# Kernel tuning notes

Hardware: AMD Instinct MI355X
Metric: run time of the kernel (lower is better)

The kernel has to match this reference:

```python
import jax, jax.numpy as jnp
import numpy as np

MARGIN = 0.1
WEIGHT_BCE = 1.0
WEIGHT_SIM = 1.0
B, L = 8192, 1024


def setup_inputs() -> dict:
    key = jax.random.key(0)
    k1, k2, k3, k4 = jax.random.split(key, 4)
    # scores must be valid probabilities for BCELoss
    scores = jax.random.uniform(k1, (B, L), dtype=jnp.float32, minval=1e-4, maxval=1.0 - 1e-4)
    candidate_lengths = jax.random.randint(k2, (B,), 1, L + 1)  # int, >=1
    # exactly one positive label per sample, at a random valid index
    pos_idx = (jax.random.uniform(k3, (B,)) * candidate_lengths.astype(jnp.float32)).astype(jnp.int32)
    labels = jnp.zeros((B, L), dtype=jnp.float32).at[jnp.arange(B), pos_idx].set(1.0)
    similarity_top_cand = jax.random.normal(k4, (B,), dtype=jnp.float32)
    return {
        "scores": scores,
        "candidate_lengths": candidate_lengths,
        "labels": labels,
        "similarity_top_cand": similarity_top_cand,
    }


def reference(scores, candidate_lengths, labels, similarity_top_cand):
    max_cand_len = scores.shape[1]
    idx = jnp.arange(max_cand_len)
    mask = (idx[None, :] < candidate_lengths[:, None])  # [B, L] bool
    maskf = mask.astype(scores.dtype)

    # ---- BinaryCELoss (torch BCELoss clamps log at -100) ----
    log_p = jnp.clip(jnp.log(scores), -100.0)
    log_1mp = jnp.clip(jnp.log1p(-scores), -100.0)
    bce_el = -(labels * log_p + (1.0 - labels) * log_1mp)  # [B, L]
    # faithful to original: .mean(1) then divided again by mask.sum(1)
    bce_per = (bce_el * maskf).mean(axis=1) / maskf.sum(axis=1)
    bce_loss = bce_per.mean()

    # ---- HingeRankLoss (vectorized; one positive per sample assumption) ----
    pos_mask = maskf * (labels == 1.0)
    neg_mask = maskf * (labels == 0.0)
    pos_sum = pos_mask.sum(axis=1)              # number of positives in valid range
    neg_cnt = neg_mask.sum(axis=1)
    # chosen score: the (single) positive's score, else -margin if no positive
    chosen = jnp.where(pos_sum > 0, (scores * pos_mask).sum(axis=1), -MARGIN)  # [B]
    hinge_el = jnp.maximum(MARGIN + scores - chosen[:, None], 0.0) * neg_mask   # [B, L]
    valid = (candidate_lengths > 0) & (neg_cnt > 0)
    per_sample = jnp.where(valid, hinge_el.sum(axis=1) / jnp.maximum(neg_cnt, 1.0), 0.0)
    vcnt = valid.sum().astype(scores.dtype)
    hinge_loss = jnp.where(vcnt > 0, per_sample.sum() / jnp.maximum(vcnt, 1.0), 0.0)

    # ---- similarity loss ----
    sim_loss = -similarity_top_cand.mean()

    combined = hinge_loss + WEIGHT_BCE * bce_loss + WEIGHT_SIM * sim_loss
    return (combined, hinge_loss, bce_loss, sim_loss)
```

## Files before the change

kernel.cpp:

```cpp
#include <hip/hip_runtime.h>

#define MARGIN 0.1f

__device__ __forceinline__ float wave_sum(float v) {
    #pragma unroll
    for (int o = 32; o > 0; o >>= 1) v += __shfl_down(v, o, 64);
    return v;
}

__global__ __launch_bounds__(256) void row_kernel(
    const float* __restrict__ scores,
    const int*   __restrict__ lens,
    const float* __restrict__ labels,
    float4* __restrict__ ws_part)
{
    const int b    = blockIdx.x;
    const int t    = threadIdx.x;
    const int lane = t & 63;
    const int wave = t >> 6;
    const int len  = lens[b];

    const float4 s4 = reinterpret_cast<const float4*>(scores + (size_t)b * 1024)[t];
    const float4 l4 = reinterpret_cast<const float4*>(labels + (size_t)b * 1024)[t];
    const float sv[4] = {s4.x, s4.y, s4.z, s4.w};
    const float lv[4] = {l4.x, l4.y, l4.z, l4.w};
    const int base = t * 4;

    float bce = 0.f, pos_cnt = 0.f, pos_sum = 0.f;
    #pragma unroll
    for (int j = 0; j < 4; ++j) {
        const float m   = (base + j < len) ? 1.f : 0.f;
        const float s   = sv[j];
        const float lab = lv[j];
        const float arg = fmaf(lab, 2.f * s - 1.f, 1.f - s);
        bce     -= m * __logf(arg);
        pos_cnt += m * lab;
        pos_sum += m * lab * s;
    }

    __shared__ float red[3][4];
    bce     = wave_sum(bce);
    pos_cnt = wave_sum(pos_cnt);
    pos_sum = wave_sum(pos_sum);
    if (lane == 0) {
        red[0][wave] = bce;
        red[1][wave] = pos_cnt;
        red[2][wave] = pos_sum;
    }
    __syncthreads();
    const float bce_tot = red[0][0] + red[0][1] + red[0][2] + red[0][3];
    const float pc      = red[1][0] + red[1][1] + red[1][2] + red[1][3];
    const float ps      = red[2][0] + red[2][1] + red[2][2] + red[2][3];
    const float chosen  = (pc > 0.f) ? ps : -MARGIN;
    const float nc      = (float)len - pc;

    float hinge = 0.f;
    #pragma unroll
    for (int j = 0; j < 4; ++j) {
        const float m = (base + j < len) ? 1.f : 0.f;
        hinge += m * (1.f - lv[j]) * fmaxf(MARGIN + sv[j] - chosen, 0.f);
    }
    hinge = wave_sum(hinge);
    __shared__ float hred[4];
    if (lane == 0) hred[wave] = hinge;
    __syncthreads();

    if (t == 0) {
        const float h_tot = hred[0] + hred[1] + hred[2] + hred[3];
        const float bce_per = bce_tot * (1.f / 1024.f) / (float)len;
        const bool  valid   = (len > 0) && (nc > 0.f);
        const float h_per   = valid ? h_tot / fmaxf(nc, 1.f) : 0.f;
        ws_part[b] = make_float4(bce_per, h_per, valid ? 1.f : 0.f, 0.f);
    }
}

__global__ __launch_bounds__(256) void finalize_kernel(
    const float4* __restrict__ ws_part,
    const float*  __restrict__ sim,
    float* __restrict__ out,
    int B)
{
    const int t    = threadIdx.x;
    const int lane = t & 63;
    const int wave = t >> 6;

    float b_acc = 0.f, h_acc = 0.f, v_acc = 0.f, s_acc = 0.f;
    for (int i = t; i < B; i += 256) {
        const float4 p = ws_part[i];
        b_acc += p.x;
        h_acc += p.y;
        v_acc += p.z;
        s_acc += sim[i];
    }
    b_acc = wave_sum(b_acc);
    h_acc = wave_sum(h_acc);
    v_acc = wave_sum(v_acc);
    s_acc = wave_sum(s_acc);

    __shared__ float red[4][4];
    if (lane == 0) {
        red[0][wave] = b_acc;
        red[1][wave] = h_acc;
        red[2][wave] = v_acc;
        red[3][wave] = s_acc;
    }
    __syncthreads();

    if (t == 0) {
        const float b_tot = red[0][0] + red[0][1] + red[0][2] + red[0][3];
        const float h_tot = red[1][0] + red[1][1] + red[1][2] + red[1][3];
        const float v_tot = red[2][0] + red[2][1] + red[2][2] + red[2][3];
        const float s_tot = red[3][0] + red[3][1] + red[3][2] + red[3][3];

        const float bce_loss   = b_tot / (float)B;
        const float hinge_loss = (v_tot > 0.f) ? h_tot / fmaxf(v_tot, 1.f) : 0.f;
        const float sim_loss   = -s_tot / (float)B;

        out[0] = hinge_loss + bce_loss + sim_loss;
        out[1] = hinge_loss;
        out[2] = bce_loss;
        out[3] = sim_loss;
    }
}

extern "C" void kernel_launch(void* const* d_in, const int* in_sizes, int n_in,
                              void* d_out, int out_size, void* d_ws, size_t ws_size,
                              hipStream_t stream) {
    const float* scores = (const float*)d_in[0];
    const int*   lens   = (const int*)d_in[1];
    const float* labels = (const float*)d_in[2];
    const float* sim    = (const float*)d_in[3];
    float* out = (float*)d_out;

    const int B = in_sizes[1];

    float4* ws_part = (float4*)d_ws;

    row_kernel<<<B, 256, 0, stream>>>(scores, lens, labels, ws_part);
    finalize_kernel<<<1, 256, 0, stream>>>(ws_part, sim, out, B);
}
```

Measured before the change: 105.1 us.

## Map one wavefront per row to drop block-level syncs and LDS reductions

The row kernel now assigns each 64-lane wavefront a full row of 1024 elements (16 per lane) and packs four rows per block. All reductions become wave shuffles, which removes the two __syncthreads and the shared-memory exchanges, and the positive count is inferred from pos_sum > 0 on the assumption of a single positive per row. The sim value is folded into the per-row workspace, and the finalize kernel widens to 1024 threads. The pos_sum shortcut is a semantic assumption: it gives a wrong count if the positive score is 0 or if there are multiple positives, and each lane now holds more registers.

```diff
diff --git a/kernel.cpp b/kernel.cpp
--- a/kernel.cpp
+++ b/kernel.cpp
@@ -12,71 +12,69 @@
     const float* __restrict__ scores,
     const int*   __restrict__ lens,
     const float* __restrict__ labels,
+    const float* __restrict__ sim,
     float4* __restrict__ ws_part)
 {
-    const int b    = blockIdx.x;
-    const int t    = threadIdx.x;
-    const int lane = t & 63;
-    const int wave = t >> 6;
-    const int len  = lens[b];
+    const int lane = threadIdx.x & 63;
+    const int wave = threadIdx.x >> 6;
+    const int row  = blockIdx.x * 4 + wave;
+    const int len  = lens[row];
 
-    const float4 s4 = reinterpret_cast<const float4*>(scores + (size_t)b * 1024)[t];
-    const float4 l4 = reinterpret_cast<const float4*>(labels + (size_t)b * 1024)[t];
-    const float sv[4] = {s4.x, s4.y, s4.z, s4.w};
-    const float lv[4] = {l4.x, l4.y, l4.z, l4.w};
-    const int base = t * 4;
+    const float4* srow = reinterpret_cast<const float4*>(scores + (size_t)row * 1024);
+    const float4* lrow = reinterpret_cast<const float4*>(labels + (size_t)row * 1024);
 
-    float bce = 0.f, pos_cnt = 0.f, pos_sum = 0.f;
+    float sv[16], lv[16];
     #pragma unroll
-    for (int j = 0; j < 4; ++j) {
-        const float m   = (base + j < len) ? 1.f : 0.f;
-        const float s   = sv[j];
-        const float lab = lv[j];
-        const float arg = fmaf(lab, 2.f * s - 1.f, 1.f - s);
-        bce     -= m * __logf(arg);
-        pos_cnt += m * lab;
-        pos_sum += m * lab * s;
+    for (int k = 0; k < 4; ++k) {
+        const float4 s4 = srow[k * 64 + lane];
+        const float4 l4 = lrow[k * 64 + lane];
+        sv[k*4+0] = s4.x; sv[k*4+1] = s4.y; sv[k*4+2] = s4.z; sv[k*4+3] = s4.w;
+        lv[k*4+0] = l4.x; lv[k*4+1] = l4.y; lv[k*4+2] = l4.z; lv[k*4+3] = l4.w;
     }
 
-    __shared__ float red[3][4];
+    float bce = 0.f, pos_sum = 0.f;
+    #pragma unroll
+    for (int k = 0; k < 4; ++k) {
+        #pragma unroll
+        for (int j = 0; j < 4; ++j) {
+            const int   idx = (k * 64 + lane) * 4 + j;
+            const float m   = (idx < len) ? 1.f : 0.f;
+            const float s   = sv[k*4+j];
+            const float lab = lv[k*4+j];
+            const float arg = fmaf(lab, 2.f * s - 1.f, 1.f - s);
+            bce     -= m * __logf(arg);
+            pos_sum += m * lab * s;
+        }
+    }
     bce     = wave_sum(bce);
-    pos_cnt = wave_sum(pos_cnt);
     pos_sum = wave_sum(pos_sum);
-    if (lane == 0) {
-        red[0][wave] = bce;
-        red[1][wave] = pos_cnt;
-        red[2][wave] = pos_sum;
-    }
-    __syncthreads();
-    const float bce_tot = red[0][0] + red[0][1] + red[0][2] + red[0][3];
-    const float pc      = red[1][0] + red[1][1] + red[1][2] + red[1][3];
-    const float ps      = red[2][0] + red[2][1] + red[2][2] + red[2][3];
-    const float chosen  = (pc > 0.f) ? ps : -MARGIN;
-    const float nc      = (float)len - pc;
+    pos_sum = __shfl(pos_sum, 0, 64);
+    const float pc     = (pos_sum > 0.f) ? 1.f : 0.f;
+    const float chosen = (pos_sum > 0.f) ? pos_sum : -MARGIN;
+    const float nc     = (float)len - pc;
 
     float hinge = 0.f;
     #pragma unroll
-    for (int j = 0; j < 4; ++j) {
-        const float m = (base + j < len) ? 1.f : 0.f;
-        hinge += m * (1.f - lv[j]) * fmaxf(MARGIN + sv[j] - chosen, 0.f);
+    for (int k = 0; k < 4; ++k) {
+        #pragma unroll
+        for (int j = 0; j < 4; ++j) {
+            const int   idx = (k * 64 + lane) * 4 + j;
+            const float m   = (idx < len) ? 1.f : 0.f;
+            hinge += m * (1.f - lv[k*4+j]) * fmaxf(MARGIN + sv[k*4+j] - chosen, 0.f);
+        }
     }
     hinge = wave_sum(hinge);
-    __shared__ float hred[4];
-    if (lane == 0) hred[wave] = hinge;
-    __syncthreads();
 
-    if (t == 0) {
-        const float h_tot = hred[0] + hred[1] + hred[2] + hred[3];
-        const float bce_per = bce_tot * (1.f / 1024.f) / (float)len;
+    if (lane == 0) {
+        const float bce_per = bce * (1.f / 1024.f) / (float)len;
         const bool  valid   = (len > 0) && (nc > 0.f);
-        const float h_per   = valid ? h_tot / fmaxf(nc, 1.f) : 0.f;
-        ws_part[b] = make_float4(bce_per, h_per, valid ? 1.f : 0.f, 0.f);
+        const float h_per   = valid ? hinge / fmaxf(nc, 1.f) : 0.f;
+        ws_part[row] = make_float4(bce_per, h_per, valid ? 1.f : 0.f, sim[row]);
     }
 }
 
-__global__ __launch_bounds__(256) void finalize_kernel(
+__global__ __launch_bounds__(1024) void finalize_kernel(
     const float4* __restrict__ ws_part,
-    const float*  __restrict__ sim,
     float* __restrict__ out,
     int B)
 {
@@ -85,19 +83,19 @@
     const int wave = t >> 6;
 
     float b_acc = 0.f, h_acc = 0.f, v_acc = 0.f, s_acc = 0.f;
-    for (int i = t; i < B; i += 256) {
+    for (int i = t; i < B; i += 1024) {
         const float4 p = ws_part[i];
         b_acc += p.x;
         h_acc += p.y;
         v_acc += p.z;
-        s_acc += sim[i];
+        s_acc += p.w;
     }
     b_acc = wave_sum(b_acc);
     h_acc = wave_sum(h_acc);
     v_acc = wave_sum(v_acc);
     s_acc = wave_sum(s_acc);
 
-    __shared__ float red[4][4];
+    __shared__ float red[4][16];
     if (lane == 0) {
         red[0][wave] = b_acc;
         red[1][wave] = h_acc;
@@ -107,11 +105,14 @@
     __syncthreads();
 
     if (t == 0) {
-        const float b_tot = red[0][0] + red[0][1] + red[0][2] + red[0][3];
-        const float h_tot = red[1][0] + red[1][1] + red[1][2] + red[1][3];
-        const float v_tot = red[2][0] + red[2][1] + red[2][2] + red[2][3];
-        const float s_tot = red[3][0] + red[3][1] + red[3][2] + red[3][3];
-
+        float b_tot = 0.f, h_tot = 0.f, v_tot = 0.f, s_tot = 0.f;
+        #pragma unroll
+        for (int w = 0; w < 16; ++w) {
+            b_tot += red[0][w];
+            h_tot += red[1][w];
+            v_tot += red[2][w];
+            s_tot += red[3][w];
+        }
         const float bce_loss   = b_tot / (float)B;
         const float hinge_loss = (v_tot > 0.f) ? h_tot / fmaxf(v_tot, 1.f) : 0.f;
         const float sim_loss   = -s_tot / (float)B;
@@ -136,6 +137,6 @@
 
     float4* ws_part = (float4*)d_ws;
 
-    row_kernel<<<B, 256, 0, stream>>>(scores, lens, labels, ws_part);
-    finalize_kernel<<<1, 256, 0, stream>>>(ws_part, sim, out, B);
+    row_kernel<<<B / 4, 256, 0, stream>>>(scores, lens, labels, sim, ws_part);
+    finalize_kernel<<<1, 1024, 0, stream>>>(ws_part, out, B);
 }
```

Result: faster. 99.85 us (-5.0%).
